# Performance work log

Measured on AMD Instinct MI355X. Metric: run time of the kernel, lower is better.

The kernel has to match this reference:

```python
import jax, jax.numpy as jnp
import numpy as np

D_MODEL = 1024
D_OUT = 64


def setup_inputs() -> dict:
    key = jax.random.key(0)
    ks = jax.random.split(key, 9)
    B, S = 4, 4096
    query = jax.random.normal(ks[0], (B, S, D_MODEL), dtype=jnp.float32)
    key_in = jax.random.normal(ks[1], (B, S, D_MODEL), dtype=jnp.float32)
    value = jax.random.normal(ks[2], (B, S, D_MODEL), dtype=jnp.float32)
    s = 1.0 / np.sqrt(D_MODEL)
    Wq = jax.random.uniform(ks[3], (D_MODEL, D_OUT), jnp.float32, -s, s)
    bq = jax.random.uniform(ks[4], (D_OUT,), jnp.float32, -s, s)
    Wk = jax.random.uniform(ks[5], (D_MODEL, D_OUT), jnp.float32, -s, s)
    bk = jax.random.uniform(ks[6], (D_OUT,), jnp.float32, -s, s)
    Wv = jax.random.uniform(ks[7], (D_MODEL, D_OUT), jnp.float32, -s, s)
    bv = jax.random.uniform(ks[8], (D_OUT,), jnp.float32, -s, s)
    return {"query": query, "key": key_in, "value": value,
            "Wq": Wq, "bq": bq, "Wk": Wk, "bk": bk, "Wv": Wv, "bv": bv}


def reference(query, key, value, Wq, bq, Wk, bk, Wv, bv):
    # Linear projections: [B,S,d_model] @ [d_model,d_out] + bias
    q = jnp.einsum('bsd,de->bse', query, Wq) + bq
    k = jnp.einsum('bsd,de->bse', key, Wk) + bk
    v = jnp.einsum('bsd,de->bse', value, Wv) + bv
    dim_k = k.shape[-1]
    # Full [B,S,S] score matrix (faithful to the unfused original)
    scores = jnp.einsum('bqe,bke->bqk', q, k) / jnp.sqrt(jnp.float32(dim_k))
    weights = jax.nn.softmax(scores, axis=-1)
    # dropout is identity in eval/inference mode
    out = jnp.einsum('bqk,bke->bqe', weights, v)
    return out
```

## Files before the change

### kernel.cpp

```cpp
#include <hip/hip_runtime.h>
#include <stdint.h>


typedef __attribute__((ext_vector_type(8))) short bf16x8;
typedef __attribute__((ext_vector_type(4))) float f32x4;

#define LOG2E_OVER8 0.1803368801111204f

__device__ __forceinline__ unsigned short f2bf(float f) {
  union { float f; uint32_t u; } v; v.f = f;
  return (unsigned short)((v.u + 0x7FFFu + ((v.u >> 16) & 1u)) >> 16);
}
__device__ __forceinline__ uint32_t f2bf2(float a, float b) {
  return (uint32_t)f2bf(a) | ((uint32_t)f2bf(b) << 16);
}

__global__ void prep_kernel(const float* __restrict__ Wq, const float* __restrict__ bq,
                            const float* __restrict__ Wk, const float* __restrict__ bk,
                            const float* __restrict__ Wv, const float* __restrict__ bv,
                            unsigned short* __restrict__ wt, float* __restrict__ bias) {
  int idx = blockIdx.x * 256 + threadIdx.x;
  int p = idx >> 16;
  int rem = idx & 65535;
  int k = rem >> 6, col = rem & 63;
  const float* W = p == 0 ? Wq : (p == 1 ? Wk : Wv);
  float scale = (p == 0) ? LOG2E_OVER8 : 1.0f;
  wt[(p << 16) + col * 1024 + k] = f2bf(W[rem] * scale);
  if (idx < 192) {
    int pp = idx >> 6, cc = idx & 63;
    const float* bsrc = pp == 0 ? bq : (pp == 1 ? bk : bv);
    bias[idx] = bsrc[cc] * ((pp == 0) ? LOG2E_OVER8 : 1.0f);
  }
}

__global__ __launch_bounds__(256, 2)
void proj_kernel(const float* __restrict__ Xq, const float* __restrict__ Xk,
                 const float* __restrict__ Xv,
                 const unsigned short* __restrict__ wt, const float* __restrict__ bias,
                 unsigned short* __restrict__ qo, unsigned short* __restrict__ ko,
                 unsigned short* __restrict__ vo) {
  __shared__ uint32_t Xs[128][36];
  __shared__ uint32_t Ws[64][36];
  const int p = blockIdx.y;
  const float* X = p == 0 ? Xq : (p == 1 ? Xk : Xv);
  const int row0 = blockIdx.x * 128;
  const int tid = threadIdx.x;
  const int wv = tid >> 6, lane = tid & 63, c = lane & 15, G = lane >> 4;
  const int srow = tid >> 1, shalf = tid & 1;
  const int wcol = tid >> 2, wq = tid & 3;

  f32x4 acc[2][4] = {};

  for (int kk = 0; kk < 1024; kk += 64) {
    {
      const float4* src = (const float4*)(X + (size_t)(row0 + srow) * 1024 + kk + shalf * 32);
      uint32_t pk[16];
#pragma unroll
      for (int i = 0; i < 8; i++) {
        float4 f = src[i];
        pk[2 * i]     = f2bf2(f.x, f.y);
        pk[2 * i + 1] = f2bf2(f.z, f.w);
      }
      uint4* dst = (uint4*)&Xs[srow][shalf * 16];
#pragma unroll
      for (int i = 0; i < 4; i++) dst[i] = ((const uint4*)pk)[i];
    }
    {
      const uint4* src = (const uint4*)(wt + (p << 16) + wcol * 1024 + kk + wq * 16);
      uint4* dst = (uint4*)&Ws[wcol][wq * 8];
      dst[0] = src[0]; dst[1] = src[1];
    }
    __syncthreads();
#pragma unroll
    for (int k2 = 0; k2 < 2; k2++) {
      bf16x8 a0 = *(const bf16x8*)((const char*)&Xs[wv * 32 + c][0]      + k2 * 64 + G * 16);
      bf16x8 a1 = *(const bf16x8*)((const char*)&Xs[wv * 32 + 16 + c][0] + k2 * 64 + G * 16);
#pragma unroll
      for (int n = 0; n < 4; n++) {
        bf16x8 bw = *(const bf16x8*)((const char*)&Ws[16 * n + c][0] + k2 * 64 + G * 16);
        acc[0][n] = __builtin_amdgcn_mfma_f32_16x16x32_bf16(a0, bw, acc[0][n], 0, 0, 0);
        acc[1][n] = __builtin_amdgcn_mfma_f32_16x16x32_bf16(a1, bw, acc[1][n], 0, 0, 0);
      }
    }
    __syncthreads();
  }
  float bcol[4];
#pragma unroll
  for (int n = 0; n < 4; n++) bcol[n] = bias[p * 64 + 16 * n + c];
  if (p < 2) {
    unsigned short* out = (p == 0) ? qo : ko;
#pragma unroll
    for (int a = 0; a < 2; a++)
#pragma unroll
      for (int n = 0; n < 4; n++)
#pragma unroll
        for (int r = 0; r < 4; r++) {
          int row = row0 + wv * 32 + a * 16 + G * 4 + r;
          out[(size_t)row * 64 + 16 * n + c] = f2bf(acc[a][n][r] + bcol[n]);
        }
  } else {
#pragma unroll
    for (int a = 0; a < 2; a++)
#pragma unroll
      for (int n = 0; n < 4; n++)
#pragma unroll
        for (int r = 0; r < 4; r++) {
          int row = row0 + wv * 32 + a * 16 + G * 4 + r;
          int bb = row >> 12, sl = row & 4095;
          int e = 16 * n + c;
          vo[((size_t)(bb * 64 + e) << 12) + sl] = f2bf(acc[a][n][r] + bcol[n]);
        }
  }
}

__global__ __launch_bounds__(512, 1)
void attn_kernel(const unsigned short* __restrict__ q_ws, const unsigned short* __restrict__ k_ws,
                 const unsigned short* __restrict__ vt_ws, float* __restrict__ out) {
  __shared__ uint32_t Ks[2][64][36];
  __shared__ uint32_t Vs[2][64][36];
  __shared__ uint32_t Pl[8][16][36];
  const int b = blockIdx.y;
  const int tid = threadIdx.x;
  const int wv = tid >> 6, lane = tid & 63, c = lane & 15, G = lane >> 4;
  const int g = wv >> 2, ws_ = wv & 3;
  const int qrow = blockIdx.x * 64 + ws_ * 16;

  bf16x8 aq[2];
#pragma unroll
  for (int k2 = 0; k2 < 2; k2++)
    aq[k2] = *(const bf16x8*)(q_ws + ((size_t)(b * 4096 + qrow + c) << 6) + k2 * 32 + G * 8);

  f32x4 o[4] = {};
  float mr[4] = {-1e30f, -1e30f, -1e30f, -1e30f};
  float lp[4] = {};

  const int gb = tid >> 8, rr = (tid >> 2) & 63, cc = tid & 3;

  for (int t = 0; t < 32; t++) {
    {
      int kv0s = gb * 2048 + t * 64;
      const uint4* ksrc = (const uint4*)(k_ws + ((size_t)(b * 4096 + kv0s + rr) << 6) + cc * 16);
      uint4* kdst = (uint4*)&Ks[gb][rr][cc * 8];
      kdst[0] = ksrc[0]; kdst[1] = ksrc[1];
      const uint4* vsrc = (const uint4*)(vt_ws + ((size_t)(b * 64 + rr) << 12) + kv0s + cc * 16);
      uint4* vdst = (uint4*)&Vs[gb][rr][cc * 8];
      vdst[0] = vsrc[0]; vdst[1] = vsrc[1];
    }
    __syncthreads();

    f32x4 sc[4] = {};
#pragma unroll
    for (int k2 = 0; k2 < 2; k2++)
#pragma unroll
      for (int f = 0; f < 4; f++) {
        bf16x8 bk = *(const bf16x8*)((const char*)&Ks[g][16 * f + c][0] + k2 * 64 + G * 16);
        sc[f] = __builtin_amdgcn_mfma_f32_16x16x32_bf16(aq[k2], bk, sc[f], 0, 0, 0);
      }

    float mn[4];
#pragma unroll
    for (int r = 0; r < 4; r++)
      mn[r] = fmaxf(fmaxf(sc[0][r], sc[1][r]), fmaxf(sc[2][r], sc[3][r]));
#pragma unroll
    for (int msk = 1; msk <= 8; msk <<= 1)
#pragma unroll
      for (int r = 0; r < 4; r++)
        mn[r] = fmaxf(mn[r], __shfl_xor(mn[r], msk));

    float pv[4][4];
#pragma unroll
    for (int r = 0; r < 4; r++) {
      float M = fmaxf(mr[r], mn[r]);
      float al = __builtin_amdgcn_exp2f(mr[r] - M);
      mr[r] = M;
      lp[r] *= al;
#pragma unroll
      for (int df = 0; df < 4; df++) o[df][r] *= al;
#pragma unroll
      for (int f = 0; f < 4; f++) pv[f][r] = __builtin_amdgcn_exp2f(sc[f][r] - M);
      lp[r] += (pv[0][r] + pv[1][r]) + (pv[2][r] + pv[3][r]);
    }

    unsigned short* plw = (unsigned short*)&Pl[wv][0][0];
#pragma unroll
    for (int f = 0; f < 4; f++)
#pragma unroll
      for (int r = 0; r < 4; r++)
        plw[(4 * G + r) * 72 + 16 * f + c] = f2bf(pv[f][r]);

    bf16x8 pa[2];
    pa[0] = *(const bf16x8*)((const char*)&Pl[wv][0][0] + c * 144 + G * 16);
    pa[1] = *(const bf16x8*)((const char*)&Pl[wv][0][0] + c * 144 + 64 + G * 16);
#pragma unroll
    for (int k2 = 0; k2 < 2; k2++)
#pragma unroll
      for (int df = 0; df < 4; df++) {
        bf16x8 bvv = *(const bf16x8*)((const char*)&Vs[g][16 * df + c][0] + k2 * 64 + G * 16);
        o[df] = __builtin_amdgcn_mfma_f32_16x16x32_bf16(pa[k2], bvv, o[df], 0, 0, 0);
      }
    __syncthreads();
  }

#pragma unroll
  for (int msk = 1; msk <= 8; msk <<= 1)
#pragma unroll
    for (int r = 0; r < 4; r++) lp[r] += __shfl_xor(lp[r], msk);

  float* Osh = (float*)&Ks[0][0][0];
  float* msh = (float*)&Vs[0][0][0];
  float* lsh = msh + 64;
  if (g == 1) {
#pragma unroll
    for (int df = 0; df < 4; df++)
#pragma unroll
      for (int r = 0; r < 4; r++)
        Osh[(ws_ * 16 + 4 * G + r) * 65 + 16 * df + c] = o[df][r];
    if (c == 0) {
#pragma unroll
      for (int r = 0; r < 4; r++) {
        msh[ws_ * 16 + 4 * G + r] = mr[r];
        lsh[ws_ * 16 + 4 * G + r] = lp[r];
      }
    }
  }
  __syncthreads();
  if (g == 0) {
#pragma unroll
    for (int r = 0; r < 4; r++) {
      int rowi = ws_ * 16 + 4 * G + r;
      float m1 = msh[rowi], l1 = lsh[rowi];
      float M = fmaxf(mr[r], m1);
      float a0 = __builtin_amdgcn_exp2f(mr[r] - M);
      float a1 = __builtin_amdgcn_exp2f(m1 - M);
      float inv = 1.0f / (a0 * lp[r] + a1 * l1);
#pragma unroll
      for (int df = 0; df < 4; df++) {
        float val = (a0 * o[df][r] + a1 * Osh[rowi * 65 + 16 * df + c]) * inv;
        out[((size_t)(b * 4096 + blockIdx.x * 64 + rowi) << 6) + 16 * df + c] = val;
      }
    }
  }
}

extern "C" void kernel_launch(void* const* d_in, const int* in_sizes, int n_in,
                              void* d_out, int out_size, void* d_ws, size_t ws_size,
                              hipStream_t stream) {
  const float* query = (const float*)d_in[0];
  const float* key   = (const float*)d_in[1];
  const float* value = (const float*)d_in[2];
  const float* Wq = (const float*)d_in[3];
  const float* bq = (const float*)d_in[4];
  const float* Wk = (const float*)d_in[5];
  const float* bk = (const float*)d_in[6];
  const float* Wv = (const float*)d_in[7];
  const float* bv = (const float*)d_in[8];

  char* ws = (char*)d_ws;
  unsigned short* q_ws  = (unsigned short*)(ws);
  unsigned short* k_ws  = (unsigned short*)(ws + (2u << 20));
  unsigned short* vt_ws = (unsigned short*)(ws + (4u << 20));
  unsigned short* wt_ws = (unsigned short*)(ws + (6u << 20));
  float* bias_ws        = (float*)(ws + (6u << 20) + 393216);

  prep_kernel<<<768, 256, 0, stream>>>(Wq, bq, Wk, bk, Wv, bv, wt_ws, bias_ws);
  proj_kernel<<<dim3(128, 3), 256, 0, stream>>>(query, key, value, wt_ws, bias_ws,
                                                q_ws, k_ws, vt_ws);
  attn_kernel<<<dim3(64, 4), 512, 0, stream>>>(q_ws, k_ws, vt_ws, (float*)d_out);
}
```

Measured before the change: 292.1 us.

## Double-buffer projection and attention tiles with direct global-to-LDS loads

Both the projection and attention kernels now stage tiles into XOR-swizzled, double-buffered LDS using global_load_lds, so the next tile's loads are issued while the current tile's MFMAs run. The projection keeps fp32 X in LDS and converts to bf16 at fragment read time, and uses smaller 64-row tiles for twice as many blocks. Attention moves to 256-thread blocks of 32 query rows with a remapped block index, again doubling the block count. The P conversion uses a cheaper rounding. These changes aim to hide memory latency and raise occupancy, at the cost of more LDS per block and slightly different bf16 rounding of P.

```diff
diff --git a/kernel.cpp b/kernel.cpp
--- a/kernel.cpp
+++ b/kernel.cpp
@@ -6,6 +6,10 @@
 typedef __attribute__((ext_vector_type(4))) float f32x4;
 
 #define LOG2E_OVER8 0.1803368801111204f
+
+#define GLOAD16(gptr, lptr)                                                            \
+  __builtin_amdgcn_global_load_lds((const __attribute__((address_space(1))) uint32_t*)(gptr), \
+                                   (__attribute__((address_space(3))) uint32_t*)(lptr), 16, 0, 0)
 
 __device__ __forceinline__ unsigned short f2bf(float f) {
   union { float f; uint32_t u; } v; v.f = f;
@@ -13,6 +17,10 @@
 }
 __device__ __forceinline__ uint32_t f2bf2(float a, float b) {
   return (uint32_t)f2bf(a) | ((uint32_t)f2bf(b) << 16);
+}
+__device__ __forceinline__ unsigned short f2bf_fast(float f) {
+  union { float f; uint32_t u; } v; v.f = f;
+  return (unsigned short)((v.u + 0x8000u) >> 16);
 }
 
 __global__ void prep_kernel(const float* __restrict__ Wq, const float* __restrict__ bq,
@@ -33,97 +41,111 @@
   }
 }
 
-__global__ __launch_bounds__(256, 2)
+__global__ __launch_bounds__(256)
 void proj_kernel(const float* __restrict__ Xq, const float* __restrict__ Xk,
                  const float* __restrict__ Xv,
                  const unsigned short* __restrict__ wt, const float* __restrict__ bias,
                  unsigned short* __restrict__ qo, unsigned short* __restrict__ ko,
                  unsigned short* __restrict__ vo) {
-  __shared__ uint32_t Xs[128][36];
-  __shared__ uint32_t Ws[64][36];
+  __shared__ float Xs[2][64][64];
+  __shared__ unsigned short Wsh[2][64][64];
   const int p = blockIdx.y;
   const float* X = p == 0 ? Xq : (p == 1 ? Xk : Xv);
-  const int row0 = blockIdx.x * 128;
+  const int row0 = blockIdx.x * 64;
   const int tid = threadIdx.x;
-  const int wv = tid >> 6, lane = tid & 63, c = lane & 15, G = lane >> 4;
-  const int srow = tid >> 1, shalf = tid & 1;
-  const int wcol = tid >> 2, wq = tid & 3;
-
-  f32x4 acc[2][4] = {};
-
+  const int lane = tid & 63, wv = tid >> 6, c = lane & 15, G = lane >> 4;
+  const int wvoff = wv * 1024;
+
+  const int xsrow = tid >> 4;
+  const int xcol = ((tid & 15) ^ xsrow) * 4;
+  const int wcolr = tid >> 3;
+  const int wkoff = ((tid & 7) ^ (wcolr & 7)) * 8;
+
+  f32x4 acc[4] = {};
+
+  auto STAGE = [&](int bufi, int kk) {
+    char* xb = (char*)&Xs[bufi][0][0];
+    char* wb = (char*)&Wsh[bufi][0][0];
+#pragma unroll
+    for (int s = 0; s < 4; s++) {
+      const float* src = X + (size_t)(row0 + s * 16 + xsrow) * 1024 + kk + xcol;
+      GLOAD16(src, xb + s * 4096 + wvoff);
+    }
+#pragma unroll
+    for (int s2 = 0; s2 < 2; s2++) {
+      const unsigned short* src = wt + (p << 16) + (size_t)(s2 * 32 + wcolr) * 1024 + kk + wkoff;
+      GLOAD16(src, wb + s2 * 4096 + wvoff);
+    }
+  };
+
+  STAGE(0, 0);
+  __syncthreads();
+  int buf = 0;
   for (int kk = 0; kk < 1024; kk += 64) {
-    {
-      const float4* src = (const float4*)(X + (size_t)(row0 + srow) * 1024 + kk + shalf * 32);
-      uint32_t pk[16];
-#pragma unroll
-      for (int i = 0; i < 8; i++) {
-        float4 f = src[i];
-        pk[2 * i]     = f2bf2(f.x, f.y);
-        pk[2 * i + 1] = f2bf2(f.z, f.w);
-      }
-      uint4* dst = (uint4*)&Xs[srow][shalf * 16];
-#pragma unroll
-      for (int i = 0; i < 4; i++) dst[i] = ((const uint4*)pk)[i];
-    }
-    {
-      const uint4* src = (const uint4*)(wt + (p << 16) + wcol * 1024 + kk + wq * 16);
-      uint4* dst = (uint4*)&Ws[wcol][wq * 8];
-      dst[0] = src[0]; dst[1] = src[1];
+    if (kk < 960) STAGE(buf ^ 1, kk + 64);
+    const char* xb = (const char*)&Xs[buf][0][0];
+    const char* wb = (const char*)&Wsh[buf][0][0];
+#pragma unroll
+    for (int k2 = 0; k2 < 2; k2++) {
+      float4 f0 = *(const float4*)(xb + (wv * 16 + c) * 256 + ((k2 * 8 + G * 2) ^ c) * 16);
+      float4 f1 = *(const float4*)(xb + (wv * 16 + c) * 256 + ((k2 * 8 + G * 2 + 1) ^ c) * 16);
+      union { uint32_t u[4]; bf16x8 v; } cv;
+      cv.u[0] = f2bf2(f0.x, f0.y); cv.u[1] = f2bf2(f0.z, f0.w);
+      cv.u[2] = f2bf2(f1.x, f1.y); cv.u[3] = f2bf2(f1.z, f1.w);
+      bf16x8 a = cv.v;
+#pragma unroll
+      for (int n = 0; n < 4; n++) {
+        bf16x8 bw = *(const bf16x8*)(wb + (16 * n + c) * 128 + (((k2 * 4 + G) ^ (c & 7)) * 16));
+        acc[n] = __builtin_amdgcn_mfma_f32_16x16x32_bf16(a, bw, acc[n], 0, 0, 0);
+      }
     }
     __syncthreads();
-#pragma unroll
-    for (int k2 = 0; k2 < 2; k2++) {
-      bf16x8 a0 = *(const bf16x8*)((const char*)&Xs[wv * 32 + c][0]      + k2 * 64 + G * 16);
-      bf16x8 a1 = *(const bf16x8*)((const char*)&Xs[wv * 32 + 16 + c][0] + k2 * 64 + G * 16);
-#pragma unroll
-      for (int n = 0; n < 4; n++) {
-        bf16x8 bw = *(const bf16x8*)((const char*)&Ws[16 * n + c][0] + k2 * 64 + G * 16);
-        acc[0][n] = __builtin_amdgcn_mfma_f32_16x16x32_bf16(a0, bw, acc[0][n], 0, 0, 0);
-        acc[1][n] = __builtin_amdgcn_mfma_f32_16x16x32_bf16(a1, bw, acc[1][n], 0, 0, 0);
-      }
-    }
-    __syncthreads();
-  }
+    buf ^= 1;
+  }
+
   float bcol[4];
 #pragma unroll
   for (int n = 0; n < 4; n++) bcol[n] = bias[p * 64 + 16 * n + c];
   if (p < 2) {
     unsigned short* out = (p == 0) ? qo : ko;
 #pragma unroll
-    for (int a = 0; a < 2; a++)
-#pragma unroll
-      for (int n = 0; n < 4; n++)
-#pragma unroll
-        for (int r = 0; r < 4; r++) {
-          int row = row0 + wv * 32 + a * 16 + G * 4 + r;
-          out[(size_t)row * 64 + 16 * n + c] = f2bf(acc[a][n][r] + bcol[n]);
-        }
+    for (int n = 0; n < 4; n++)
+#pragma unroll
+      for (int r = 0; r < 4; r++) {
+        int row = row0 + wv * 16 + G * 4 + r;
+        out[(size_t)row * 64 + 16 * n + c] = f2bf(acc[n][r] + bcol[n]);
+      }
   } else {
 #pragma unroll
-    for (int a = 0; a < 2; a++)
-#pragma unroll
-      for (int n = 0; n < 4; n++)
-#pragma unroll
-        for (int r = 0; r < 4; r++) {
-          int row = row0 + wv * 32 + a * 16 + G * 4 + r;
-          int bb = row >> 12, sl = row & 4095;
-          int e = 16 * n + c;
-          vo[((size_t)(bb * 64 + e) << 12) + sl] = f2bf(acc[a][n][r] + bcol[n]);
-        }
-  }
-}
-
-__global__ __launch_bounds__(512, 1)
+    for (int n = 0; n < 4; n++)
+#pragma unroll
+      for (int r = 0; r < 4; r++) {
+        int row = row0 + wv * 16 + G * 4 + r;
+        int bb = row >> 12, sl = row & 4095;
+        int e = 16 * n + c;
+        vo[((size_t)(bb * 64 + e) << 12) + sl] = f2bf(acc[n][r] + bcol[n]);
+      }
+  }
+}
+
+__global__ __launch_bounds__(256)
 void attn_kernel(const unsigned short* __restrict__ q_ws, const unsigned short* __restrict__ k_ws,
                  const unsigned short* __restrict__ vt_ws, float* __restrict__ out) {
-  __shared__ uint32_t Ks[2][64][36];
-  __shared__ uint32_t Vs[2][64][36];
-  __shared__ uint32_t Pl[8][16][36];
-  const int b = blockIdx.y;
+  __shared__ unsigned short Ks[2][2][64][64];
+  __shared__ unsigned short Vs[2][2][64][64];
+  __shared__ uint32_t Pl[4][16][36];
+  __shared__ float msh[2][16], lsh[2][16];
+  const int bid = blockIdx.x;
+  const int b = (bid & 7) >> 1;
+  const int xt = ((bid >> 3) << 1) | (bid & 1);
   const int tid = threadIdx.x;
-  const int wv = tid >> 6, lane = tid & 63, c = lane & 15, G = lane >> 4;
-  const int g = wv >> 2, ws_ = wv & 3;
-  const int qrow = blockIdx.x * 64 + ws_ * 16;
+  const int lane = tid & 63, wv = tid >> 6, c = lane & 15, G = lane >> 4;
+  const int ws_ = wv & 1, g = wv >> 1;
+  const int qrow = xt * 32 + ws_ * 16;
+  const int wvoff = wv * 1024;
+
+  const int srow = tid >> 3;
+  const int scol = ((tid & 7) ^ (srow & 7)) * 8;
 
   bf16x8 aq[2];
 #pragma unroll
@@ -134,26 +156,36 @@
   float mr[4] = {-1e30f, -1e30f, -1e30f, -1e30f};
   float lp[4] = {};
 
-  const int gb = tid >> 8, rr = (tid >> 2) & 63, cc = tid & 3;
-
+  auto STAGE = [&](int bufi, int t) {
+#pragma unroll
+    for (int gb = 0; gb < 2; gb++) {
+      int kv0 = gb * 2048 + t * 64;
+      char* kb = (char*)&Ks[bufi][gb][0][0];
+      char* vb = (char*)&Vs[bufi][gb][0][0];
+#pragma unroll
+      for (int h = 0; h < 2; h++) {
+        const unsigned short* ksrc = k_ws + ((size_t)(b * 4096 + kv0 + h * 32 + srow) << 6) + scol;
+        GLOAD16(ksrc, kb + h * 4096 + wvoff);
+        const unsigned short* vsrc = vt_ws + ((size_t)(b * 64 + h * 32 + srow) << 12) + kv0 + scol;
+        GLOAD16(vsrc, vb + h * 4096 + wvoff);
+      }
+    }
+  };
+
+  STAGE(0, 0);
+  __syncthreads();
+  int buf = 0;
   for (int t = 0; t < 32; t++) {
-    {
-      int kv0s = gb * 2048 + t * 64;
-      const uint4* ksrc = (const uint4*)(k_ws + ((size_t)(b * 4096 + kv0s + rr) << 6) + cc * 16);
-      uint4* kdst = (uint4*)&Ks[gb][rr][cc * 8];
-      kdst[0] = ksrc[0]; kdst[1] = ksrc[1];
-      const uint4* vsrc = (const uint4*)(vt_ws + ((size_t)(b * 64 + rr) << 12) + kv0s + cc * 16);
-      uint4* vdst = (uint4*)&Vs[gb][rr][cc * 8];
-      vdst[0] = vsrc[0]; vdst[1] = vsrc[1];
-    }
-    __syncthreads();
+    if (t < 31) STAGE(buf ^ 1, t + 1);
+    const char* kb = (const char*)&Ks[buf][g][0][0];
+    const char* vb = (const char*)&Vs[buf][g][0][0];
 
     f32x4 sc[4] = {};
 #pragma unroll
     for (int k2 = 0; k2 < 2; k2++)
 #pragma unroll
       for (int f = 0; f < 4; f++) {
-        bf16x8 bk = *(const bf16x8*)((const char*)&Ks[g][16 * f + c][0] + k2 * 64 + G * 16);
+        bf16x8 bk = *(const bf16x8*)(kb + (16 * f + c) * 128 + (((k2 * 4 + G) ^ (c & 7)) * 16));
         sc[f] = __builtin_amdgcn_mfma_f32_16x16x32_bf16(aq[k2], bk, sc[f], 0, 0, 0);
       }
 
@@ -186,7 +218,7 @@
     for (int f = 0; f < 4; f++)
 #pragma unroll
       for (int r = 0; r < 4; r++)
-        plw[(4 * G + r) * 72 + 16 * f + c] = f2bf(pv[f][r]);
+        plw[(4 * G + r) * 72 + 16 * f + c] = f2bf_fast(pv[f][r]);
 
     bf16x8 pa[2];
     pa[0] = *(const bf16x8*)((const char*)&Pl[wv][0][0] + c * 144 + G * 16);
@@ -195,10 +227,11 @@
     for (int k2 = 0; k2 < 2; k2++)
 #pragma unroll
       for (int df = 0; df < 4; df++) {
-        bf16x8 bvv = *(const bf16x8*)((const char*)&Vs[g][16 * df + c][0] + k2 * 64 + G * 16);
+        bf16x8 bvv = *(const bf16x8*)(vb + (16 * df + c) * 128 + (((k2 * 4 + G) ^ (c & 7)) * 16));
         o[df] = __builtin_amdgcn_mfma_f32_16x16x32_bf16(pa[k2], bvv, o[df], 0, 0, 0);
       }
     __syncthreads();
+    buf ^= 1;
   }
 
 #pragma unroll
@@ -206,9 +239,7 @@
 #pragma unroll
     for (int r = 0; r < 4; r++) lp[r] += __shfl_xor(lp[r], msk);
 
-  float* Osh = (float*)&Ks[0][0][0];
-  float* msh = (float*)&Vs[0][0][0];
-  float* lsh = msh + 64;
+  float* Osh = (float*)&Ks[0][0][0][0];
   if (g == 1) {
 #pragma unroll
     for (int df = 0; df < 4; df++)
@@ -218,8 +249,8 @@
     if (c == 0) {
 #pragma unroll
       for (int r = 0; r < 4; r++) {
-        msh[ws_ * 16 + 4 * G + r] = mr[r];
-        lsh[ws_ * 16 + 4 * G + r] = lp[r];
+        msh[ws_][4 * G + r] = mr[r];
+        lsh[ws_][4 * G + r] = lp[r];
       }
     }
   }
@@ -227,16 +258,16 @@
   if (g == 0) {
 #pragma unroll
     for (int r = 0; r < 4; r++) {
-      int rowi = ws_ * 16 + 4 * G + r;
-      float m1 = msh[rowi], l1 = lsh[rowi];
+      int rowi = 4 * G + r;
+      float m1 = msh[ws_][rowi], l1 = lsh[ws_][rowi];
       float M = fmaxf(mr[r], m1);
       float a0 = __builtin_amdgcn_exp2f(mr[r] - M);
       float a1 = __builtin_amdgcn_exp2f(m1 - M);
       float inv = 1.0f / (a0 * lp[r] + a1 * l1);
 #pragma unroll
       for (int df = 0; df < 4; df++) {
-        float val = (a0 * o[df][r] + a1 * Osh[rowi * 65 + 16 * df + c]) * inv;
-        out[((size_t)(b * 4096 + blockIdx.x * 64 + rowi) << 6) + 16 * df + c] = val;
+        float val = (a0 * o[df][r] + a1 * Osh[(ws_ * 16 + rowi) * 65 + 16 * df + c]) * inv;
+        out[((size_t)(b * 4096 + qrow + rowi) << 6) + 16 * df + c] = val;
       }
     }
   }
@@ -263,7 +294,7 @@
   float* bias_ws        = (float*)(ws + (6u << 20) + 393216);
 
   prep_kernel<<<768, 256, 0, stream>>>(Wq, bq, Wk, bk, Wv, bv, wt_ws, bias_ws);
-  proj_kernel<<<dim3(128, 3), 256, 0, stream>>>(query, key, value, wt_ws, bias_ws,
+  proj_kernel<<<dim3(256, 3), 256, 0, stream>>>(query, key, value, wt_ws, bias_ws,
                                                 q_ws, k_ws, vt_ws);
-  attn_kernel<<<dim3(64, 4), 512, 0, stream>>>(q_ws, k_ws, vt_ws, (float*)d_out);
-}
+  attn_kernel<<<512, 256, 0, stream>>>(q_ws, k_ws, vt_ws, (float*)d_out);
+}
```

After: 286.3 us. 2.0% less time.
